# Kernel optimization log

Hardware: AMD Instinct MI355X
Metric: run time of the kernel (lower is better)

Reference implementation:

```python
import jax, jax.numpy as jnp
import numpy as np

SEMANTIC_DIM = 128
N_COMPONENTS = 2
EMBED_DIM = SEMANTIC_DIM * N_COMPONENTS  # 256
MAX_LEN = 512


def sinusoidal_pe(max_len, d_model):
    pos = jnp.arange(max_len, dtype=jnp.float32)[:, None]              # (L,1)
    div = jnp.exp(jnp.arange(0, d_model, 2, dtype=jnp.float32) * (-np.log(10000.0) / d_model))
    ang = pos * div                                                     # (L, d/2)
    # interleave sin/cos: pe[:,0::2]=sin, pe[:,1::2]=cos
    return jnp.stack([jnp.sin(ang), jnp.cos(ang)], axis=-1).reshape(max_len, d_model)


def setup_inputs() -> dict:
    key = jax.random.key(0)
    k1, k2, k3, k4 = jax.random.split(key, 4)
    byte_sequence = jax.random.randint(k1, (64, 512), 0, 256, dtype=jnp.int64)
    continuous_positions = jax.random.uniform(k2, (64, 2048), dtype=jnp.float32)
    emb_table = jax.random.normal(k3, (256, EMBED_DIM), dtype=jnp.float32)
    locality_shapes = jax.random.normal(k4, (256, 3), dtype=jnp.float32)
    return {
        "byte_sequence": byte_sequence,
        "continuous_positions": continuous_positions,
        "emb_table": emb_table,
        "locality_shapes": locality_shapes,
    }


def reference(byte_sequence, continuous_positions, emb_table, locality_shapes):
    B, L = byte_sequence.shape
    pe = sinusoidal_pe(MAX_LEN, EMBED_DIM)[:L]                          # (L, E)
    byte_embeds = emb_table[byte_sequence] + pe[None, :, :]             # (B, L, E)
    byte_amplitudes = byte_embeds.reshape(B, L, N_COMPONENTS, SEMANTIC_DIM)

    byte_positions = jnp.linspace(0.0, 1.0, L, dtype=jnp.float32)      # (L,)
    x_diff = continuous_positions[:, :, None] - byte_positions[None, None, :]  # (B, P, L)

    lp = locality_shapes[byte_sequence]                                 # (B, L, 3)
    widths = jnp.abs(lp[:, :, 1]) * 0.02 + 1e-5                         # (B, L)
    amplitudes = jax.nn.sigmoid(lp[:, :, 2])                            # (B, L)

    local_basis = jnp.exp(-0.5 * (x_diff / widths[:, None, :]) ** 2) * amplitudes[:, None, :]
    semantic_field = jnp.einsum('bpl,blcd->bpcd', local_basis, byte_amplitudes)
    return semantic_field
```

## Files before the change

kernel.cpp:

```cpp
#include <hip/hip_runtime.h>
#include <math.h>

#define LSEQ 512
#define EDIM 256
#define PDIM 2048
#define BM   128
#define BK   32
#define NT   16

typedef _Float16 f16x8 __attribute__((ext_vector_type(8)));
typedef float    f32x4 __attribute__((ext_vector_type(4)));

__device__ __host__ inline int tile_off(int r, int g) {
    return ((r >> 1) << 6) + ((r & 1) << 5) + (((g ^ ((r >> 1) & 3)) & 3) << 3);
}

__device__ inline void g2lds16(const void* g, void* l) {
    __builtin_amdgcn_global_load_lds(
        (const __attribute__((address_space(1))) void*)g,
        (__attribute__((address_space(3))) void*)l, 16, 0, 0);
}

__global__ void precompute_tables(const float* __restrict__ ls,
                                  const int* __restrict__ bs,
                                  float* __restrict__ pe,
                                  float2* __restrict__ params, int nparams) {
    const int bid = blockIdx.x, tid = threadIdx.x;
    if (bid < LSEQ) {
        if (tid < 128) {
            float div = expf((2.0f * (float)tid) * (-logf(10000.0f) / 256.0f));
            float ang = (float)bid * div;
            pe[bid * EDIM + 2 * tid]     = sinf(ang);
            pe[bid * EDIM + 2 * tid + 1] = cosf(ang);
        }
    } else {
        const int i = (bid - LSEQ) * 256 + tid;
        if (i < nparams) {
            const int byte = bs[i];
            const float l1 = ls[byte * 3 + 1];
            const float l2 = ls[byte * 3 + 2];
            const float wdt = fabsf(l1) * 0.02f + 1e-5f;
            params[i] = make_float2(-0.5f / (wdt * wdt),
                                    1.0f / (1.0f + __expf(-l2)));
        }
    }
}

__global__ void precompute_baset(const int* __restrict__ bs,
                                 const float* __restrict__ emb,
                                 const float* __restrict__ pe,
                                 _Float16* __restrict__ baset) {
    const int b = blockIdx.x >> 4;
    const int t = blockIdx.x & 15;
    const int e = threadIdx.x;
    const int* bsb = bs + b * LSEQ + t * BK;
    _Float16* chunk = baset + ((size_t)(b * NT + t) << 13);
#pragma unroll
    for (int g = 0; g < 4; ++g) {
        f16x8 v;
#pragma unroll
        for (int j = 0; j < 8; ++j) {
            const int l = t * BK + g * 8 + j;
            const int byte = bsb[g * 8 + j];
            v[j] = (_Float16)(emb[byte * EDIM + e] + pe[l * EDIM + e]);
        }
        *(f16x8*)&chunk[tile_off(e, g)] = v;
    }
}

__global__ __launch_bounds__(512, 4) void field_mfma(
    const float*    __restrict__ cpos,
    const float2*   __restrict__ params,
    const _Float16* __restrict__ baset,
    float*          __restrict__ out) {

    __shared__ __align__(16) _Float16 sW[2][BM * BK];
    __shared__ __align__(16) _Float16 sB[2][EDIM * BK];
    __shared__ __align__(16) float2   sPrm[LSEQ];

    const int orig = blockIdx.x;
    const int wg   = (orig & 7) * 128 + (orig >> 3);
    const int b    = wg >> 4;
    const int pt   = wg & 15;

    const int tid = threadIdx.x, lane = tid & 63, wave = tid >> 6;
    const int c15 = lane & 15, g4 = lane >> 4;
    const int wrow = wave >> 2, wcol = wave & 3;

    const int sp = tid >> 2;
    const int sg = tid & 3;
    const float mypos = cpos[b * PDIM + pt * BM + sp];
    const float invL  = 1.0f / (float)(LSEQ - 1);
    const int   woff  = tile_off(sp, sg);

    int aoff[4], boff[4];
#pragma unroll
    for (int rt = 0; rt < 4; ++rt) aoff[rt] = tile_off(wrow * 64 + rt * 16 + c15, g4);
#pragma unroll
    for (int ct = 0; ct < 4; ++ct) boff[ct] = tile_off(wcol * 64 + ct * 16 + c15, g4);

    sPrm[tid] = params[b * LSEQ + tid];
    const _Float16* bt = baset + ((size_t)b * NT << 13);
#pragma unroll
    for (int buf = 0; buf < 2; ++buf) {
        const _Float16* src = bt + buf * 8192 + wave * 1024 + lane * 8;
        g2lds16(src,       &sB[buf][wave * 1024]);
        g2lds16(src + 512, &sB[buf][wave * 1024 + 512]);
    }
    __syncthreads();

    auto genW = [&](int t, int dbuf) {
        const float4* qp = (const float4*)&sPrm[t * BK + sg * 8];
        const float4 q01 = qp[0], q23 = qp[1], q45 = qp[2], q67 = qp[3];
        const float bl0 = (float)(t * BK + sg * 8) * invL;
        f16x8 wv;
#define GENW(i, c2, am) { float d = mypos - (bl0 + (float)(i) * invL); \
                          wv[i] = (_Float16)((am) * __expf(d * d * (c2))); }
        GENW(0, q01.x, q01.y) GENW(1, q01.z, q01.w)
        GENW(2, q23.x, q23.y) GENW(3, q23.z, q23.w)
        GENW(4, q45.x, q45.y) GENW(5, q45.z, q45.w)
        GENW(6, q67.x, q67.y) GENW(7, q67.z, q67.w)
#undef GENW
        *(f16x8*)&sW[dbuf][woff] = wv;
    };

    genW(0, 0);
    __syncthreads();

    f32x4 acc[4][4];
#pragma unroll
    for (int i = 0; i < 4; ++i)
#pragma unroll
        for (int j = 0; j < 4; ++j) acc[i][j] = (f32x4)(0.f);

    for (int t = 0; t < NT; ++t) {
        const int cur = t & 1;
        if (t < NT - 1) genW(t + 1, cur ^ 1);

        const _Float16* wb = sW[cur];
        const _Float16* bb = sB[cur];
        f16x8 af[4];
#pragma unroll
        for (int rt = 0; rt < 4; ++rt) af[rt] = *(const f16x8*)&wb[aoff[rt]];
        __builtin_amdgcn_s_setprio(1);
#pragma unroll
        for (int ct = 0; ct < 4; ++ct) {
            const f16x8 bf = *(const f16x8*)&bb[boff[ct]];
#pragma unroll
            for (int rt = 0; rt < 4; ++rt)
                acc[rt][ct] = __builtin_amdgcn_mfma_f32_16x16x32_f16(af[rt], bf, acc[rt][ct], 0, 0, 0);
        }
        __builtin_amdgcn_s_setprio(0);

        __syncthreads();

        if (t < NT - 2) {
            const _Float16* src = bt + (t + 2) * 8192 + wave * 1024 + lane * 8;
            g2lds16(src,       &sB[cur][wave * 1024]);
            g2lds16(src + 512, &sB[cur][wave * 1024 + 512]);
        }
    }

#pragma unroll
    for (int rt = 0; rt < 4; ++rt)
#pragma unroll
        for (int ct = 0; ct < 4; ++ct) {
            const int e = wcol * 64 + ct * 16 + c15;
#pragma unroll
            for (int r = 0; r < 4; ++r) {
                const int p = pt * BM + wrow * 64 + rt * 16 + g4 * 4 + r;
                out[((size_t)b * PDIM + p) * EDIM + e] = acc[rt][ct][r];
            }
        }
}

extern "C" void kernel_launch(void* const* d_in, const int* in_sizes, int n_in,
                              void* d_out, int out_size, void* d_ws, size_t ws_size,
                              hipStream_t stream) {
    const int*   bs   = (const int*)d_in[0];
    const float* cpos = (const float*)d_in[1];
    const float* emb  = (const float*)d_in[2];
    const float* ls   = (const float*)d_in[3];

    const int B = in_sizes[0] / LSEQ;

    char* ws = (char*)d_ws;
    float*    pe     = (float*)ws;
    float2*   params = (float2*)(ws + (1u << 19));
    _Float16* baset  = (_Float16*)(ws + (1u << 20));

    const int nparams = B * LSEQ;
    precompute_tables<<<LSEQ + (nparams + 255) / 256, 256, 0, stream>>>(ls, bs, pe, params, nparams);
    precompute_baset<<<B * NT, 256, 0, stream>>>(bs, emb, pe, baset);
    field_mfma<<<B * (PDIM / BM), 512, 0, stream>>>(cpos, params, baset, (float*)d_out);
}
```

Before: 73.96 us.

## Fuse precompute kernels and fold amplitude into exp2 for weight generation

```diff
diff --git a/kernel.cpp b/kernel.cpp
--- a/kernel.cpp
+++ b/kernel.cpp
@@ -9,7 +9,22 @@
 #define NT   16
 
 typedef _Float16 f16x8 __attribute__((ext_vector_type(8)));
+typedef _Float16 f16x2 __attribute__((ext_vector_type(2)));
 typedef float    f32x4 __attribute__((ext_vector_type(4)));
+
+#if __has_builtin(__builtin_amdgcn_exp2f)
+#define EXP2F(x) __builtin_amdgcn_exp2f(x)
+#else
+#define EXP2F(x) __expf((x) * 0.6931471805599453f)
+#endif
+
+__device__ inline f16x2 pk2(float a, float b) {
+#if __has_builtin(__builtin_amdgcn_cvt_pkrtz)
+    return __builtin_bit_cast(f16x2, __builtin_amdgcn_cvt_pkrtz(a, b));
+#else
+    f16x2 r; r[0] = (_Float16)a; r[1] = (_Float16)b; return r;
+#endif
+}
 
 __device__ __host__ inline int tile_off(int r, int g) {
     return ((r >> 1) << 6) + ((r & 1) << 5) + (((g ^ ((r >> 1) & 3)) & 3) << 3);
@@ -21,50 +36,43 @@
         (__attribute__((address_space(3))) void*)l, 16, 0, 0);
 }
 
-__global__ void precompute_tables(const float* __restrict__ ls,
-                                  const int* __restrict__ bs,
-                                  float* __restrict__ pe,
-                                  float2* __restrict__ params, int nparams) {
-    const int bid = blockIdx.x, tid = threadIdx.x;
-    if (bid < LSEQ) {
-        if (tid < 128) {
-            float div = expf((2.0f * (float)tid) * (-logf(10000.0f) / 256.0f));
-            float ang = (float)bid * div;
-            pe[bid * EDIM + 2 * tid]     = sinf(ang);
-            pe[bid * EDIM + 2 * tid + 1] = cosf(ang);
-        }
-    } else {
-        const int i = (bid - LSEQ) * 256 + tid;
-        if (i < nparams) {
-            const int byte = bs[i];
-            const float l1 = ls[byte * 3 + 1];
-            const float l2 = ls[byte * 3 + 2];
-            const float wdt = fabsf(l1) * 0.02f + 1e-5f;
-            params[i] = make_float2(-0.5f / (wdt * wdt),
-                                    1.0f / (1.0f + __expf(-l2)));
-        }
-    }
-}
-
-__global__ void precompute_baset(const int* __restrict__ bs,
-                                 const float* __restrict__ emb,
-                                 const float* __restrict__ pe,
-                                 _Float16* __restrict__ baset) {
-    const int b = blockIdx.x >> 4;
-    const int t = blockIdx.x & 15;
-    const int e = threadIdx.x;
-    const int* bsb = bs + b * LSEQ + t * BK;
-    _Float16* chunk = baset + ((size_t)(b * NT + t) << 13);
+__global__ __launch_bounds__(256) void precompute_all(
+    const int*   __restrict__ bs,
+    const float* __restrict__ ls,
+    const float* __restrict__ emb,
+    float2*      __restrict__ params,
+    _Float16*    __restrict__ baset) {
+    const int b   = blockIdx.x >> 4;
+    const int t   = blockIdx.x & 15;
+    const int tid = threadIdx.x;
+
+    __shared__ int sByte[BK];
+    if (tid < BK) {
+        const int l    = t * BK + tid;
+        const int byte = bs[b * LSEQ + l];
+        sByte[tid] = byte;
+        const float l1  = ls[byte * 3 + 1];
+        const float l2  = ls[byte * 3 + 2];
+        const float wdt = fabsf(l1) * 0.02f + 1e-5f;
+        const float amp = 1.0f / (1.0f + __expf(-l2));
+        params[b * LSEQ + l] = make_float2(-0.72134752f / (wdt * wdt),
+                                           __log2f(amp));
+    }
+    __syncthreads();
+
+    const float div = __expf((float)(tid >> 1) * (-2.0f * 9.210340372f / 256.0f));
+    _Float16* chunk = baset + ((size_t)blockIdx.x << 13);
 #pragma unroll
     for (int g = 0; g < 4; ++g) {
         f16x8 v;
 #pragma unroll
         for (int j = 0; j < 8; ++j) {
-            const int l = t * BK + g * 8 + j;
-            const int byte = bsb[g * 8 + j];
-            v[j] = (_Float16)(emb[byte * EDIM + e] + pe[l * EDIM + e]);
-        }
-        *(f16x8*)&chunk[tile_off(e, g)] = v;
+            const int lj  = g * 8 + j;
+            const float ang = (float)(t * BK + lj) * div;
+            const float pev = (tid & 1) ? cosf(ang) : sinf(ang);
+            v[j] = (_Float16)(emb[sByte[lj] * EDIM + tid] + pev);
+        }
+        *(f16x8*)&chunk[tile_off(tid, g)] = v;
     }
 }
 
@@ -113,14 +121,19 @@
         const float4* qp = (const float4*)&sPrm[t * BK + sg * 8];
         const float4 q01 = qp[0], q23 = qp[1], q45 = qp[2], q67 = qp[3];
         const float bl0 = (float)(t * BK + sg * 8) * invL;
+        float w[8];
+#define GW(i, c2, la) { float d = mypos - (bl0 + (float)(i) * invL); \
+                        w[i] = EXP2F(fmaf(d * d, (c2), (la))); }
+        GW(0, q01.x, q01.y) GW(1, q01.z, q01.w)
+        GW(2, q23.x, q23.y) GW(3, q23.z, q23.w)
+        GW(4, q45.x, q45.y) GW(5, q45.z, q45.w)
+        GW(6, q67.x, q67.y) GW(7, q67.z, q67.w)
+#undef GW
         f16x8 wv;
-#define GENW(i, c2, am) { float d = mypos - (bl0 + (float)(i) * invL); \
-                          wv[i] = (_Float16)((am) * __expf(d * d * (c2))); }
-        GENW(0, q01.x, q01.y) GENW(1, q01.z, q01.w)
-        GENW(2, q23.x, q23.y) GENW(3, q23.z, q23.w)
-        GENW(4, q45.x, q45.y) GENW(5, q45.z, q45.w)
-        GENW(6, q67.x, q67.y) GENW(7, q67.z, q67.w)
-#undef GENW
+        ((f16x2*)&wv)[0] = pk2(w[0], w[1]);
+        ((f16x2*)&wv)[1] = pk2(w[2], w[3]);
+        ((f16x2*)&wv)[2] = pk2(w[4], w[5]);
+        ((f16x2*)&wv)[3] = pk2(w[6], w[7]);
         *(f16x8*)&sW[dbuf][woff] = wv;
     };
 
@@ -185,12 +198,9 @@
     const int B = in_sizes[0] / LSEQ;
 
     char* ws = (char*)d_ws;
-    float*    pe     = (float*)ws;
-    float2*   params = (float2*)(ws + (1u << 19));
-    _Float16* baset  = (_Float16*)(ws + (1u << 20));
-
-    const int nparams = B * LSEQ;
-    precompute_tables<<<LSEQ + (nparams + 255) / 256, 256, 0, stream>>>(ls, bs, pe, params, nparams);
-    precompute_baset<<<B * NT, 256, 0, stream>>>(bs, emb, pe, baset);
+    float2*   params = (float2*)ws;
+    _Float16* baset  = (_Float16*)(ws + (1u << 18));
+
+    precompute_all<<<B * NT, 256, 0, stream>>>(bs, ls, emb, params, baset);
     field_mfma<<<B * (PDIM / BM), 512, 0, stream>>>(cpos, params, baset, (float*)d_out);
 }
```

Measured after the change: 65.99 us. 10.8% less time.
